# Kernel optimization log

Hardware: AMD Instinct MI355X
Metric: run time of the kernel (lower is better)

Reference implementation:

```python
import jax, jax.numpy as jnp
import numpy as np

LN_EPS = 1e-6
IGNORE_INDEX = -100

D_MODEL = 768
VOCAB = 32128
B, S = 4, 512


def setup_inputs() -> dict:
    key = jax.random.key(0)
    k1, k2, k3 = jax.random.split(key, 3)
    hidden_states = jax.random.normal(k1, (B, S, D_MODEL), dtype=jnp.float32)
    labels = jax.random.randint(k2, (B, S), 0, VOCAB, dtype=jnp.int64)
    ln_weight = jnp.ones((D_MODEL,), dtype=jnp.float32)
    # nn.Linear(d_model, vocab, bias=False).weight has shape [vocab, d_model]
    lm_head_weight = jax.random.normal(k3, (VOCAB, D_MODEL), dtype=jnp.float32) * (D_MODEL ** -0.5)
    return {
        "hidden_states": hidden_states,
        "labels": labels,
        "ln_weight": ln_weight,
        "lm_head_weight": lm_head_weight,
    }


def t5_layer_norm(x, weight, eps=LN_EPS):
    # T5-style RMSNorm: no mean subtraction, variance in fp32
    variance = jnp.mean(x.astype(jnp.float32) ** 2, axis=-1, keepdims=True)
    x = x * jax.lax.rsqrt(variance + eps)
    return weight * x


def reference(hidden_states, labels, ln_weight, lm_head_weight):
    h = t5_layer_norm(hidden_states, ln_weight)
    # dropout is identity in eval / rate=0
    # lm_head: [B,S,D] @ [V,D]^T -> [B,S,V]
    prediction_scores = jnp.einsum("bsd,vd->bsv", h, lm_head_weight)
    # CrossEntropyLoss(ignore_index=-100), mean over non-ignored tokens
    logits = prediction_scores.reshape(-1, VOCAB)  # [B*S, V]
    flat_labels = labels.reshape(-1)
    valid = flat_labels != IGNORE_INDEX
    safe_labels = jnp.where(valid, flat_labels, 0)
    logp = jax.nn.log_softmax(logits, axis=-1)
    nll = -jnp.take_along_axis(logp, safe_labels[:, None], axis=-1)[:, 0]
    nll = jnp.where(valid, nll, 0.0)
    loss = jnp.sum(nll) / jnp.maximum(jnp.sum(valid.astype(jnp.float32)), 1.0)
    return (loss, prediction_scores)
```

## Files before the change

kernel.cpp:

```cpp
#include <hip/hip_runtime.h>
#include <stdint.h>

#define DM 768
#define VOC 32128
#define NTOK 2048
#define NBY (VOC / 128)
#define IGN (-100)

typedef __bf16 bf16x8 __attribute__((ext_vector_type(8)));
typedef float f32x4 __attribute__((ext_vector_type(4)));

typedef __attribute__((address_space(1))) void gvoid_t;
typedef __attribute__((address_space(3))) void svoid_t;

__device__ __forceinline__ void gl_lds16(const void* g, void* s) {
  __builtin_amdgcn_global_load_lds((gvoid_t*)g, (svoid_t*)s, 16, 0, 0);
}

__device__ __forceinline__ unsigned short f2bf(float f) {
  unsigned int u = __float_as_uint(f);
  u = (u + 0x7fffu + ((u >> 16) & 1u)) >> 16;
  return (unsigned short)u;
}

__global__ void __launch_bounds__(256) cvt_w_kernel(const float* __restrict__ W,
                                                    unsigned short* __restrict__ Wb) {
  size_t i = ((size_t)blockIdx.x * 256 + threadIdx.x) * 4;
  float4 v = *(const float4*)(W + i);
  ushort4 o;
  o.x = f2bf(v.x); o.y = f2bf(v.y); o.z = f2bf(v.z); o.w = f2bf(v.w);
  *(ushort4*)(Wb + i) = o;
}

__global__ void __launch_bounds__(256) rmsnorm_kernel(const float* __restrict__ x,
                                                      const float* __restrict__ w,
                                                      unsigned short* __restrict__ h) {
  int tok = blockIdx.x;
  const float* xr = x + (size_t)tok * DM;
  int t = threadIdx.x;
  float v0 = xr[t], v1 = xr[t + 256], v2 = xr[t + 512];
  float ss = v0 * v0 + v1 * v1 + v2 * v2;
  for (int off = 32; off; off >>= 1) ss += __shfl_down(ss, off);
  __shared__ float red[4];
  int wv = t >> 6, ln = t & 63;
  if (ln == 0) red[wv] = ss;
  __syncthreads();
  float tot = red[0] + red[1] + red[2] + red[3];
  float inv = rsqrtf(tot * (1.0f / DM) + 1e-6f);
  unsigned short* hr = h + (size_t)tok * DM;
  hr[t]       = f2bf(v0 * inv * w[t]);
  hr[t + 256] = f2bf(v1 * inv * w[t + 256]);
  hr[t + 512] = f2bf(v2 * inv * w[t + 512]);
}

__global__ void __launch_bounds__(256, 2) gemm_kernel(const unsigned short* __restrict__ A,
                                                      const unsigned short* __restrict__ Bw,
                                                      float* __restrict__ C,
                                                      float* __restrict__ Pm,
                                                      float* __restrict__ Ps) {
  __shared__ __align__(16) unsigned short As[128 * 32];
  __shared__ __align__(16) unsigned short Bs[128 * 32];

  const int m0 = blockIdx.x * 128;
  const int n0 = blockIdx.y * 128;
  const int by = blockIdx.y;
  const int tid = threadIdx.x;
  const int wv = tid >> 6, ln = tid & 63;
  const int srow = ln >> 2;
  const int scol = ((ln & 3) ^ ((srow >> 1) & 3)) * 8;

  const unsigned short* aSrc0 = A + (size_t)(m0 + wv * 32 + srow) * DM + scol;
  const unsigned short* aSrc1 = aSrc0 + (size_t)16 * DM;
  const unsigned short* bSrc0 = Bw + (size_t)(n0 + wv * 32 + srow) * DM + scol;
  const unsigned short* bSrc1 = bSrc0 + (size_t)16 * DM;
  unsigned short* aDst0 = &As[(wv * 32) * 32];
  unsigned short* aDst1 = &As[(wv * 32 + 16) * 32];
  unsigned short* bDst0 = &Bs[(wv * 32) * 32];
  unsigned short* bDst1 = &Bs[(wv * 32 + 16) * 32];

  const int quad = ln >> 4, l15 = ln & 15;
  const int slot = (quad ^ ((l15 >> 1) & 3)) * 8;
  const int wr = (wv >> 1) * 64;
  const int wc = (wv & 1) * 64;

  f32x4 acc[4][4];
#pragma unroll
  for (int i = 0; i < 4; ++i)
#pragma unroll
    for (int j = 0; j < 4; ++j) {
      acc[i][j][0] = 0.f; acc[i][j][1] = 0.f; acc[i][j][2] = 0.f; acc[i][j][3] = 0.f;
    }

  for (int kt = 0; kt < 24; ++kt) {
    const int ko = kt * 32;
    gl_lds16(aSrc0 + ko, aDst0);
    gl_lds16(aSrc1 + ko, aDst1);
    gl_lds16(bSrc0 + ko, bDst0);
    gl_lds16(bSrc1 + ko, bDst1);
    __syncthreads();

    bf16x8 af[4], bfv[4];
#pragma unroll
    for (int i = 0; i < 4; ++i) {
      af[i]  = *(const bf16x8*)(As + (wr + i * 16 + l15) * 32 + slot);
      bfv[i] = *(const bf16x8*)(Bs + (wc + i * 16 + l15) * 32 + slot);
    }
#pragma unroll
    for (int mi = 0; mi < 4; ++mi)
#pragma unroll
      for (int ni = 0; ni < 4; ++ni)
        acc[mi][ni] = __builtin_amdgcn_mfma_f32_16x16x32_bf16(af[mi], bfv[ni], acc[mi][ni], 0, 0, 0);
    __syncthreads();
  }

#pragma unroll
  for (int mi = 0; mi < 4; ++mi) {
#pragma unroll
    for (int r = 0; r < 4; ++r) {
      const int row = m0 + wr + mi * 16 + quad * 4 + r;
      float* cp = C + (size_t)row * VOC + (n0 + wc + l15);
#pragma unroll
      for (int ni = 0; ni < 4; ++ni)
        __builtin_nontemporal_store(acc[mi][ni][r], cp + ni * 16);
    }
  }

  float* pmL = (float*)As;
  float* psL = (float*)Bs;
  float rm[4][4], rs[4][4];
#pragma unroll
  for (int mi = 0; mi < 4; ++mi) {
#pragma unroll
    for (int r = 0; r < 4; ++r) {
      float m = fmaxf(fmaxf(acc[mi][0][r], acc[mi][1][r]),
                      fmaxf(acc[mi][2][r], acc[mi][3][r]));
#pragma unroll
      for (int off = 1; off < 16; off <<= 1) m = fmaxf(m, __shfl_xor(m, off));
      float s = __expf(acc[mi][0][r] - m) + __expf(acc[mi][1][r] - m) +
                __expf(acc[mi][2][r] - m) + __expf(acc[mi][3][r] - m);
#pragma unroll
      for (int off = 1; off < 16; off <<= 1) s += __shfl_xor(s, off);
      rm[mi][r] = m; rs[mi][r] = s;
    }
  }
  __syncthreads();
  if (l15 == 0) {
#pragma unroll
    for (int mi = 0; mi < 4; ++mi)
#pragma unroll
      for (int r = 0; r < 4; ++r) {
        int row = wr + mi * 16 + quad * 4 + r;
        pmL[(wv & 1) * 128 + row] = rm[mi][r];
        psL[(wv & 1) * 128 + row] = rs[mi][r];
      }
  }
  __syncthreads();
  if (tid < 128) {
    float ma = pmL[tid], mb = pmL[128 + tid];
    float nm = fmaxf(ma, mb);
    float S = psL[tid] * __expf(ma - nm) + psL[128 + tid] * __expf(mb - nm);
    Pm[(size_t)by * NTOK + m0 + tid] = nm;
    Ps[(size_t)by * NTOK + m0 + tid] = S;
  }
}

__global__ void __launch_bounds__(256) loss_finalize_kernel(const float* __restrict__ Pm,
                                                            const float* __restrict__ Ps,
                                                            const float* __restrict__ scores,
                                                            const int* __restrict__ labels,
                                                            float* __restrict__ nll) {
  const int tok = blockIdx.x;
  float m = -1e30f, s = 0.f;
  for (int j = threadIdx.x; j < NBY; j += 256) {
    float m2 = Pm[(size_t)j * NTOK + tok], s2 = Ps[(size_t)j * NTOK + tok];
    float nm = fmaxf(m, m2);
    s = s * __expf(m - nm) + s2 * __expf(m2 - nm);
    m = nm;
  }
  for (int off = 32; off; off >>= 1) {
    float m2 = __shfl_down(m, off), s2 = __shfl_down(s, off);
    float nm = fmaxf(m, m2);
    s = s * __expf(m - nm) + s2 * __expf(m2 - nm);
    m = nm;
  }
  __shared__ float ms[4], sh[4];
  int wv = threadIdx.x >> 6, ln = threadIdx.x & 63;
  if (ln == 0) { ms[wv] = m; sh[wv] = s; }
  __syncthreads();
  if (threadIdx.x == 0) {
    float M = ms[0], S = sh[0];
    for (int i = 1; i < 4; ++i) {
      float nm = fmaxf(M, ms[i]);
      S = S * __expf(M - nm) + sh[i] * __expf(ms[i] - nm);
      M = nm;
    }
    int lab = labels[tok];
    float v = 0.f;
    if (lab != IGN) v = (M + logf(S)) - scores[(size_t)tok * VOC + lab];
    nll[tok] = v;
  }
}

__global__ void __launch_bounds__(256) reduce_kernel(const float* __restrict__ nll,
                                                     const int* __restrict__ labels,
                                                     float* __restrict__ out) {
  float s = 0.f, c = 0.f;
  for (int i = threadIdx.x; i < NTOK; i += 256) {
    s += nll[i];
    c += (labels[i] != IGN) ? 1.0f : 0.0f;
  }
  for (int off = 32; off; off >>= 1) { s += __shfl_down(s, off); c += __shfl_down(c, off); }
  __shared__ float rs[4], rc[4];
  int wv = threadIdx.x >> 6, ln = threadIdx.x & 63;
  if (ln == 0) { rs[wv] = s; rc[wv] = c; }
  __syncthreads();
  if (threadIdx.x == 0) {
    float S = rs[0] + rs[1] + rs[2] + rs[3];
    float Cc = rc[0] + rc[1] + rc[2] + rc[3];
    out[0] = S / fmaxf(Cc, 1.0f);
  }
}

extern "C" void kernel_launch(void* const* d_in, const int* in_sizes, int n_in,
                              void* d_out, int out_size, void* d_ws, size_t ws_size,
                              hipStream_t stream) {
  const float* hs     = (const float*)d_in[0];
  const int*   labels = (const int*)d_in[1];
  const float* lnw    = (const float*)d_in[2];
  const float* W      = (const float*)d_in[3];

  float* out    = (float*)d_out;
  float* scores = out + 1;

  char* ws = (char*)d_ws;
  unsigned short* Wb = (unsigned short*)ws;                 ws += (size_t)VOC * DM * 2;
  unsigned short* Hb = (unsigned short*)ws;                 ws += (size_t)NTOK * DM * 2;
  float* Pm          = (float*)ws;                          ws += (size_t)NBY * NTOK * 4;
  float* Ps          = (float*)ws;                          ws += (size_t)NBY * NTOK * 4;
  float* nll         = (float*)ws;

  cvt_w_kernel<<<(VOC * DM / 4) / 256, 256, 0, stream>>>(W, Wb);
  rmsnorm_kernel<<<NTOK, 256, 0, stream>>>(hs, lnw, Hb);
  gemm_kernel<<<dim3(NTOK / 128, VOC / 128), 256, 0, stream>>>(Hb, Wb, scores, Pm, Ps);
  loss_finalize_kernel<<<NTOK, 256, 0, stream>>>(Pm, Ps, scores, labels, nll);
  reduce_kernel<<<1, 256, 0, stream>>>(nll, labels, out);
}
```

Measured before the change: 477.9 us.

## Restructure GEMM to 256x128 tiles with triple-buffered LDS pipeline and tile swizzle

New measurement: 473.1 us. About the same (-1.0%).

```diff
diff --git a/kernel.cpp b/kernel.cpp
--- a/kernel.cpp
+++ b/kernel.cpp
@@ -53,35 +53,45 @@
   hr[t + 512] = f2bf(v2 * inv * w[t + 512]);
 }
 
-__global__ void __launch_bounds__(256, 2) gemm_kernel(const unsigned short* __restrict__ A,
+#define TILE_ELEMS 24576
+#define A_ELEMS    16384
+
+__global__ void __launch_bounds__(512, 2) gemm_kernel(const unsigned short* __restrict__ A,
                                                       const unsigned short* __restrict__ Bw,
                                                       float* __restrict__ C,
                                                       float* __restrict__ Pm,
                                                       float* __restrict__ Ps) {
-  __shared__ __align__(16) unsigned short As[128 * 32];
-  __shared__ __align__(16) unsigned short Bs[128 * 32];
-
-  const int m0 = blockIdx.x * 128;
-  const int n0 = blockIdx.y * 128;
-  const int by = blockIdx.y;
-  const int tid = threadIdx.x;
-  const int wv = tid >> 6, ln = tid & 63;
-  const int srow = ln >> 2;
-  const int scol = ((ln & 3) ^ ((srow >> 1) & 3)) * 8;
-
-  const unsigned short* aSrc0 = A + (size_t)(m0 + wv * 32 + srow) * DM + scol;
-  const unsigned short* aSrc1 = aSrc0 + (size_t)16 * DM;
-  const unsigned short* bSrc0 = Bw + (size_t)(n0 + wv * 32 + srow) * DM + scol;
-  const unsigned short* bSrc1 = bSrc0 + (size_t)16 * DM;
-  unsigned short* aDst0 = &As[(wv * 32) * 32];
-  unsigned short* aDst1 = &As[(wv * 32 + 16) * 32];
-  unsigned short* bDst0 = &Bs[(wv * 32) * 32];
-  unsigned short* bDst1 = &Bs[(wv * 32 + 16) * 32];
-
-  const int quad = ln >> 4, l15 = ln & 15;
-  const int slot = (quad ^ ((l15 >> 1) & 3)) * 8;
-  const int wr = (wv >> 1) * 64;
-  const int wc = (wv & 1) * 64;
+  __shared__ __align__(16) unsigned short LDS[3 * TILE_ELEMS];
+
+  const int id = blockIdx.x;
+  const int w  = (id & 7) * 251 + (id >> 3);
+  const int by = w >> 3;
+  const int m0 = (w & 7) * 256;
+  const int n0 = by * 128;
+
+  const int tid  = threadIdx.x;
+  const int wv   = tid >> 6, ln = tid & 63;
+  const int l15  = ln & 15, quad = ln >> 4;
+  const int wvm  = wv >> 1;
+  const int wvn  = wv & 1;
+
+  const int lr  = ln >> 3;
+  const int qsw = ((ln & 7) ^ lr) * 8;
+  const unsigned short* aS = A  + (size_t)(m0 + wv * 32 + lr) * DM + qsw;
+  const unsigned short* bS = Bw + (size_t)(n0 + wv * 16 + lr) * DM + qsw;
+  const int aDof = wv * 32 * 64;
+  const int bDof = A_ELEMS + wv * 16 * 64;
+
+  auto STAGE = [&](unsigned short* sb, int kt) {
+    const unsigned short* a = aS + kt * 64;
+    const unsigned short* b = bS + kt * 64;
+    unsigned short* ad = sb + aDof;
+    unsigned short* bd = sb + bDof;
+#pragma unroll
+    for (int c = 0; c < 4; ++c) gl_lds16(a + (size_t)c * (8 * DM), ad + c * 512);
+#pragma unroll
+    for (int c = 0; c < 2; ++c) gl_lds16(b + (size_t)c * (8 * DM), bd + c * 512);
+  };
 
   f32x4 acc[4][4];
 #pragma unroll
@@ -91,42 +101,63 @@
       acc[i][j][0] = 0.f; acc[i][j][1] = 0.f; acc[i][j][2] = 0.f; acc[i][j][3] = 0.f;
     }
 
-  for (int kt = 0; kt < 24; ++kt) {
-    const int ko = kt * 32;
-    gl_lds16(aSrc0 + ko, aDst0);
-    gl_lds16(aSrc1 + ko, aDst1);
-    gl_lds16(bSrc0 + ko, bDst0);
-    gl_lds16(bSrc1 + ko, bDst1);
-    __syncthreads();
-
-    bf16x8 af[4], bfv[4];
-#pragma unroll
-    for (int i = 0; i < 4; ++i) {
-      af[i]  = *(const bf16x8*)(As + (wr + i * 16 + l15) * 32 + slot);
-      bfv[i] = *(const bf16x8*)(Bs + (wc + i * 16 + l15) * 32 + slot);
-    }
-#pragma unroll
-    for (int mi = 0; mi < 4; ++mi)
-#pragma unroll
-      for (int ni = 0; ni < 4; ++ni)
-        acc[mi][ni] = __builtin_amdgcn_mfma_f32_16x16x32_bf16(af[mi], bfv[ni], acc[mi][ni], 0, 0, 0);
-    __syncthreads();
-  }
+  const int sw = l15 & 7;
+  auto COMPUTE = [&](const unsigned short* At) {
+    const unsigned short* Bt = At + A_ELEMS;
+#pragma unroll
+    for (int kk = 0; kk < 2; ++kk) {
+      const int so = ((kk * 4 + quad) ^ sw) * 8;
+      bf16x8 a[4], b[4];
+#pragma unroll
+      for (int i = 0; i < 4; ++i) {
+        a[i] = *(const bf16x8*)(At + (wvm * 64 + i * 16 + l15) * 64 + so);
+        b[i] = *(const bf16x8*)(Bt + (wvn * 64 + i * 16 + l15) * 64 + so);
+      }
+      __builtin_amdgcn_s_setprio(1);
+#pragma unroll
+      for (int mi = 0; mi < 4; ++mi)
+#pragma unroll
+        for (int ni = 0; ni < 4; ++ni)
+          acc[mi][ni] = __builtin_amdgcn_mfma_f32_16x16x32_bf16(a[mi], b[ni], acc[mi][ni], 0, 0, 0);
+      __builtin_amdgcn_s_setprio(0);
+    }
+  };
+
+  unsigned short* p0 = LDS;
+  unsigned short* p1 = LDS + TILE_ELEMS;
+  unsigned short* p2 = LDS + 2 * TILE_ELEMS;
+
+  STAGE(p0, 0);
+  STAGE(p1, 1);
+  asm volatile("s_waitcnt vmcnt(6)" ::: "memory");
+  __builtin_amdgcn_s_barrier();
+
+  for (int t = 0; t < 10; ++t) {
+    STAGE(p2, t + 2);
+    COMPUTE(p0);
+    asm volatile("s_waitcnt vmcnt(6)" ::: "memory");
+    __builtin_amdgcn_s_barrier();
+    unsigned short* tmp = p0; p0 = p1; p1 = p2; p2 = tmp;
+  }
+  COMPUTE(p0);
+  asm volatile("s_waitcnt vmcnt(0)" ::: "memory");
+  __builtin_amdgcn_s_barrier();
+  COMPUTE(p1);
 
 #pragma unroll
   for (int mi = 0; mi < 4; ++mi) {
 #pragma unroll
     for (int r = 0; r < 4; ++r) {
-      const int row = m0 + wr + mi * 16 + quad * 4 + r;
-      float* cp = C + (size_t)row * VOC + (n0 + wc + l15);
+      const int row = m0 + wvm * 64 + mi * 16 + quad * 4 + r;
+      float* cp = C + (size_t)row * VOC + (n0 + wvn * 64 + l15);
 #pragma unroll
       for (int ni = 0; ni < 4; ++ni)
         __builtin_nontemporal_store(acc[mi][ni][r], cp + ni * 16);
     }
   }
 
-  float* pmL = (float*)As;
-  float* psL = (float*)Bs;
+  float* pmL = (float*)LDS;
+  float* psL = pmL + 512;
   float rm[4][4], rs[4][4];
 #pragma unroll
   for (int mi = 0; mi < 4; ++mi) {
@@ -143,22 +174,21 @@
       rm[mi][r] = m; rs[mi][r] = s;
     }
   }
-  __syncthreads();
   if (l15 == 0) {
 #pragma unroll
     for (int mi = 0; mi < 4; ++mi)
 #pragma unroll
       for (int r = 0; r < 4; ++r) {
-        int row = wr + mi * 16 + quad * 4 + r;
-        pmL[(wv & 1) * 128 + row] = rm[mi][r];
-        psL[(wv & 1) * 128 + row] = rs[mi][r];
+        int rr = wvm * 64 + mi * 16 + quad * 4 + r;
+        pmL[wvn * 256 + rr] = rm[mi][r];
+        psL[wvn * 256 + rr] = rs[mi][r];
       }
   }
   __syncthreads();
-  if (tid < 128) {
-    float ma = pmL[tid], mb = pmL[128 + tid];
+  if (tid < 256) {
+    float ma = pmL[tid], mb = pmL[256 + tid];
     float nm = fmaxf(ma, mb);
-    float S = psL[tid] * __expf(ma - nm) + psL[128 + tid] * __expf(mb - nm);
+    float S = psL[tid] * __expf(ma - nm) + psL[256 + tid] * __expf(mb - nm);
     Pm[(size_t)by * NTOK + m0 + tid] = nm;
     Ps[(size_t)by * NTOK + m0 + tid] = S;
   }
@@ -241,7 +271,7 @@
 
   cvt_w_kernel<<<(VOC * DM / 4) / 256, 256, 0, stream>>>(W, Wb);
   rmsnorm_kernel<<<NTOK, 256, 0, stream>>>(hs, lnw, Hb);
-  gemm_kernel<<<dim3(NTOK / 128, VOC / 128), 256, 0, stream>>>(Hb, Wb, scores, Pm, Ps);
+  gemm_kernel<<<8 * NBY, 512, 0, stream>>>(Hb, Wb, scores, Pm, Ps);
   loss_finalize_kernel<<<NTOK, 256, 0, stream>>>(Pm, Ps, scores, labels, nll);
   reduce_kernel<<<1, 256, 0, stream>>>(nll, labels, out);
 }
```

## Fuse fp32-to-bf16 weight conversion into GEMM B-tile loads and remap block order

Applied to the files above, without the earlier changes.

Measured after the change: 516.9 us. 1.08x slower.

```diff
diff --git a/kernel.cpp b/kernel.cpp
--- a/kernel.cpp
+++ b/kernel.cpp
@@ -21,15 +21,6 @@
   unsigned int u = __float_as_uint(f);
   u = (u + 0x7fffu + ((u >> 16) & 1u)) >> 16;
   return (unsigned short)u;
-}
-
-__global__ void __launch_bounds__(256) cvt_w_kernel(const float* __restrict__ W,
-                                                    unsigned short* __restrict__ Wb) {
-  size_t i = ((size_t)blockIdx.x * 256 + threadIdx.x) * 4;
-  float4 v = *(const float4*)(W + i);
-  ushort4 o;
-  o.x = f2bf(v.x); o.y = f2bf(v.y); o.z = f2bf(v.z); o.w = f2bf(v.w);
-  *(ushort4*)(Wb + i) = o;
 }
 
 __global__ void __launch_bounds__(256) rmsnorm_kernel(const float* __restrict__ x,
@@ -54,16 +45,19 @@
 }
 
 __global__ void __launch_bounds__(256, 2) gemm_kernel(const unsigned short* __restrict__ A,
-                                                      const unsigned short* __restrict__ Bw,
+                                                      const float* __restrict__ W,
                                                       float* __restrict__ C,
                                                       float* __restrict__ Pm,
                                                       float* __restrict__ Ps) {
   __shared__ __align__(16) unsigned short As[128 * 32];
   __shared__ __align__(16) unsigned short Bs[128 * 32];
 
-  const int m0 = blockIdx.x * 128;
-  const int n0 = blockIdx.y * 128;
-  const int by = blockIdx.y;
+  const int id = blockIdx.x;
+  const int w  = (id & 7) * 502 + (id >> 3);
+  const int by = w >> 4;
+  const int m0 = (w & 15) * 128;
+  const int n0 = by * 128;
+
   const int tid = threadIdx.x;
   const int wv = tid >> 6, ln = tid & 63;
   const int srow = ln >> 2;
@@ -71,12 +65,15 @@
 
   const unsigned short* aSrc0 = A + (size_t)(m0 + wv * 32 + srow) * DM + scol;
   const unsigned short* aSrc1 = aSrc0 + (size_t)16 * DM;
-  const unsigned short* bSrc0 = Bw + (size_t)(n0 + wv * 32 + srow) * DM + scol;
-  const unsigned short* bSrc1 = bSrc0 + (size_t)16 * DM;
   unsigned short* aDst0 = &As[(wv * 32) * 32];
   unsigned short* aDst1 = &As[(wv * 32 + 16) * 32];
-  unsigned short* bDst0 = &Bs[(wv * 32) * 32];
-  unsigned short* bDst1 = &Bs[(wv * 32 + 16) * 32];
+
+  const int br  = ln >> 1;
+  const int kh  = (ln & 1) * 16;
+  const float* wSrc = W + (size_t)(n0 + wv * 32 + br) * DM + kh;
+  const int bsw = (br >> 1) & 3;
+  unsigned short* bDst0 = &Bs[(wv * 32 + br) * 32 + (((kh >> 3) + 0) ^ bsw) * 8];
+  unsigned short* bDst1 = &Bs[(wv * 32 + br) * 32 + (((kh >> 3) + 1) ^ bsw) * 8];
 
   const int quad = ln >> 4, l15 = ln & 15;
   const int slot = (quad ^ ((l15 >> 1) & 3)) * 8;
@@ -93,10 +90,25 @@
 
   for (int kt = 0; kt < 24; ++kt) {
     const int ko = kt * 32;
+    float4 b0 = *(const float4*)(wSrc + ko);
+    float4 b1 = *(const float4*)(wSrc + ko + 4);
+    float4 b2 = *(const float4*)(wSrc + ko + 8);
+    float4 b3 = *(const float4*)(wSrc + ko + 12);
     gl_lds16(aSrc0 + ko, aDst0);
     gl_lds16(aSrc1 + ko, aDst1);
-    gl_lds16(bSrc0 + ko, bDst0);
-    gl_lds16(bSrc1 + ko, bDst1);
+    unsigned int p0, p1, p2, p3, p4, p5, p6, p7;
+    asm("v_cvt_pk_bf16_f32 %0, %1, %2" : "=v"(p0) : "v"(b0.x), "v"(b0.y));
+    asm("v_cvt_pk_bf16_f32 %0, %1, %2" : "=v"(p1) : "v"(b0.z), "v"(b0.w));
+    asm("v_cvt_pk_bf16_f32 %0, %1, %2" : "=v"(p2) : "v"(b1.x), "v"(b1.y));
+    asm("v_cvt_pk_bf16_f32 %0, %1, %2" : "=v"(p3) : "v"(b1.z), "v"(b1.w));
+    asm("v_cvt_pk_bf16_f32 %0, %1, %2" : "=v"(p4) : "v"(b2.x), "v"(b2.y));
+    asm("v_cvt_pk_bf16_f32 %0, %1, %2" : "=v"(p5) : "v"(b2.z), "v"(b2.w));
+    asm("v_cvt_pk_bf16_f32 %0, %1, %2" : "=v"(p6) : "v"(b3.x), "v"(b3.y));
+    asm("v_cvt_pk_bf16_f32 %0, %1, %2" : "=v"(p7) : "v"(b3.z), "v"(b3.w));
+    uint4 w0; w0.x = p0; w0.y = p1; w0.z = p2; w0.w = p3;
+    uint4 w1; w1.x = p4; w1.y = p5; w1.z = p6; w1.w = p7;
+    *(uint4*)bDst0 = w0;
+    *(uint4*)bDst1 = w1;
     __syncthreads();
 
     bf16x8 af[4], bfv[4];
@@ -233,15 +245,13 @@
   float* scores = out + 1;
 
   char* ws = (char*)d_ws;
-  unsigned short* Wb = (unsigned short*)ws;                 ws += (size_t)VOC * DM * 2;
   unsigned short* Hb = (unsigned short*)ws;                 ws += (size_t)NTOK * DM * 2;
   float* Pm          = (float*)ws;                          ws += (size_t)NBY * NTOK * 4;
   float* Ps          = (float*)ws;                          ws += (size_t)NBY * NTOK * 4;
   float* nll         = (float*)ws;
 
-  cvt_w_kernel<<<(VOC * DM / 4) / 256, 256, 0, stream>>>(W, Wb);
   rmsnorm_kernel<<<NTOK, 256, 0, stream>>>(hs, lnw, Hb);
-  gemm_kernel<<<dim3(NTOK / 128, VOC / 128), 256, 0, stream>>>(Hb, Wb, scores, Pm, Ps);
+  gemm_kernel<<<16 * NBY, 256, 0, stream>>>(Hb, W, scores, Pm, Ps);
   loss_finalize_kernel<<<NTOK, 256, 0, stream>>>(Pm, Ps, scores, labels, nll);
   reduce_kernel<<<1, 256, 0, stream>>>(nll, labels, out);
 }
```
